# Optimization experiments

Hardware: AMD Instinct MI355X
Metric: run time of the kernel (lower is better)

Reference implementation:

```python
import jax, jax.numpy as jnp
import numpy as np
import math

B, T, C = 2, 1024, 1024
NEMBD = 1024
NATTN = 1024
NHEAD = 16
CTX = 1024
HS = NATTN // NHEAD          # head size = 64
ROT = HS // 2                # rotary dims = 32


def rotate_half(x):
    x1, x2 = x[..., : x.shape[-1] // 2], x[..., x.shape[-1] // 2 :]
    return jnp.concatenate((-x2, x1), axis=-1)


def setup_inputs() -> dict:
    key = jax.random.key(0)
    ks = jax.random.split(key, 16)
    s = 0.02
    inp = {
        "x": jax.random.normal(ks[0], (B, T, C), dtype=jnp.float32),
        # time-decay params (torch inits them to ones; add noise for a nontrivial test)
        "time_w": 1.0 + s * jax.random.normal(ks[1], (NHEAD, CTX), dtype=jnp.float32),
        "time_alpha": 1.0 + s * jax.random.normal(ks[2], (NHEAD, 1, CTX), dtype=jnp.float32),
        "time_beta": 1.0 + s * jax.random.normal(ks[3], (NHEAD, CTX, 1), dtype=jnp.float32),
        "time_gamma": 1.0 + s * jax.random.normal(ks[4], (CTX, 1), dtype=jnp.float32),
        # projections (stored as (in, out) for x @ W)
        "Wq": s * jax.random.normal(ks[5], (NEMBD, NATTN), dtype=jnp.float32),
        "bq": s * jax.random.normal(ks[6], (NATTN,), dtype=jnp.float32),
        "Wk": s * jax.random.normal(ks[7], (NEMBD, NATTN), dtype=jnp.float32),
        "bk": s * jax.random.normal(ks[8], (NATTN,), dtype=jnp.float32),
        "Wv": s * jax.random.normal(ks[9], (NEMBD, NATTN), dtype=jnp.float32),
        "bv": s * jax.random.normal(ks[10], (NATTN,), dtype=jnp.float32),
        # 1x1 conv over head channels: (out_head, in_head)
        "Wmix": s * jax.random.normal(ks[11], (NHEAD, NHEAD), dtype=jnp.float32),
        "Wo": s * jax.random.normal(ks[12], (NATTN, NEMBD), dtype=jnp.float32),
        "bo": s * jax.random.normal(ks[13], (NEMBD,), dtype=jnp.float32),
    }
    return inp


def reference(x, time_w, time_alpha, time_beta, time_gamma,
              Wq, bq, Wk, bk, Wv, bv, Wmix, Wo, bo):
    Bx, Tx, Cx = x.shape
    TT = CTX

    # --- relative time-decay weight matrix (H, T, T) ---
    w = jnp.pad(time_w, ((0, 0), (0, TT)))          # (H, 2TT)
    w = jnp.tile(w, (1, TT))                        # (H, 2TT*TT)
    w = w[:, :-TT].reshape(NHEAD, TT, 2 * TT - 1)
    w = w[:, :, TT - 1:]                            # (H, TT, TT)
    w = w[:, :Tx, :Tx] * time_alpha[:, :, :Tx] * time_beta[:, :Tx, :]

    # --- time shift of the first half of channels ---
    half = Cx // 2
    x_shift = jnp.pad(x[:, :, :half], ((0, 0), (1, 0), (0, 0)))[:, :Tx, :]
    xs = jnp.concatenate([x_shift, x[:, :, half:]], axis=-1)

    # --- q/k/v projections -> (B, H, T, hs) ---
    q = (xs @ Wq + bq).reshape(Bx, Tx, NHEAD, HS).transpose(0, 2, 1, 3)
    k = (xs @ Wk + bk).reshape(Bx, Tx, NHEAD, HS).transpose(0, 2, 1, 3)
    v = (xs @ Wv + bv).reshape(Bx, Tx, NHEAD, HS).transpose(0, 2, 1, 3)

    # --- rotary on the first ROT dims of each head (base = ctx_len) ---
    qr, q_pass = q[..., :ROT], q[..., ROT:]
    kr, k_pass = k[..., :ROT], k[..., ROT:]
    inv_freq = 1.0 / (jnp.float32(CTX) ** (jnp.arange(0, ROT, 2, dtype=jnp.float32) / ROT))
    t = jnp.arange(Tx, dtype=jnp.float32)
    freqs = t[:, None] * inv_freq[None, :]          # (T, ROT/2)
    emb = jnp.concatenate((freqs, freqs), axis=-1)  # (T, ROT)
    cos, sin = jnp.cos(emb), jnp.sin(emb)
    qr = qr * cos + rotate_half(qr) * sin
    kr = kr * cos + rotate_half(kr) * sin
    q = jnp.concatenate((qr, q_pass), axis=-1)
    k = jnp.concatenate((kr, k_pass), axis=-1)

    # --- attention with time decay and cross-head 1x1 mix ---
    att = jnp.einsum('bhtd,bhsd->bhts', q, k) * (1.0 / math.sqrt(HS))
    att = jax.nn.softmax(att, axis=-1)
    att = att * w[None]                              # (B,H,T,T) * (1,H,T,T)
    att = jnp.einsum('gh,bhts->bgts', Wmix, att)     # 1x1 conv over head channel
    y = jnp.einsum('bhts,bhsd->bhtd', att, v)
    y = y.transpose(0, 2, 1, 3).reshape(Bx, Tx, NATTN)
    return (y @ Wo + bo) * time_gamma[:Tx, :]
```

## Files before the change

kernel.cpp:

```cpp
#include <hip/hip_runtime.h>

typedef unsigned short u16;
typedef unsigned int u32;
typedef __attribute__((ext_vector_type(8))) short bf16x8;
typedef __attribute__((ext_vector_type(4))) float f32x4;

#define MFMA(a,b,c) __builtin_amdgcn_mfma_f32_16x16x32_bf16(a,b,c,0,0,0)

__device__ __forceinline__ float b2f(u16 u){
  union { unsigned int i; float f; } v; v.i = ((unsigned int)u)<<16; return v.f;
}
__device__ __forceinline__ u16 f2b(float f){
  union { float f; unsigned int i; } v; v.f = f;
  unsigned int r = (v.i + 0x7FFFu + ((v.i>>16)&1u))>>16;
  return (u16)r;
}
__device__ __forceinline__ void gld16(const u16* g, u16* l){
  __builtin_amdgcn_global_load_lds((const __attribute__((address_space(1))) u32*)g,
                                   (__attribute__((address_space(3))) u32*)l, 16, 0, 0);
}

__global__ __launch_bounds__(256) void k_pre(
    const float* __restrict__ x,
    const float* __restrict__ Wq, const float* __restrict__ Wk,
    const float* __restrict__ Wv, const float* __restrict__ Wo,
    u16* __restrict__ xs, u16* __restrict__ WT, u16* __restrict__ WoT)
{
  int bid = blockIdx.x;
  int tid = threadIdx.x;
  if (bid < 1024){
    int idx = bid*256 + tid;
    size_t e = (size_t)idx*8;
    int c = (int)(e & 1023);
    int t = (int)((e>>10)&1023);
    float4 f0 = {0.f,0.f,0.f,0.f}, f1 = {0.f,0.f,0.f,0.f};
    const float* src = nullptr;
    if (c < 512){ if (t > 0) src = x + e - 1024; }
    else        { src = x + e; }
    if (src){ f0 = *(const float4*)src; f1 = *(const float4*)(src+4); }
    u16 o[8];
    o[0]=f2b(f0.x); o[1]=f2b(f0.y); o[2]=f2b(f0.z); o[3]=f2b(f0.w);
    o[4]=f2b(f1.x); o[5]=f2b(f1.y); o[6]=f2b(f1.z); o[7]=f2b(f1.w);
    *(uint4*)(xs + e) = *(const uint4*)o;
    return;
  }
  int z  = (bid-1024)>>8;
  int rc = (bid-1024)&255;
  const float* src = (z==0)?Wq:((z==1)?Wk:((z==2)?Wv:Wo));
  u16* dst = (z==3)? WoT : (WT + (size_t)z*1048576);
  int c0 = (rc&15)*64, r0 = (rc>>4)*64;
  __shared__ u16 tile[64][72];
  int r = tid>>2, cc = (tid&3)*16;
  const float* sp = src + (size_t)(r0+r)*1024 + c0+cc;
  float4 a0 = *(const float4*)(sp);
  float4 a1 = *(const float4*)(sp+4);
  float4 a2 = *(const float4*)(sp+8);
  float4 a3 = *(const float4*)(sp+12);
  tile[r][cc+0]=f2b(a0.x); tile[r][cc+1]=f2b(a0.y); tile[r][cc+2]=f2b(a0.z); tile[r][cc+3]=f2b(a0.w);
  tile[r][cc+4]=f2b(a1.x); tile[r][cc+5]=f2b(a1.y); tile[r][cc+6]=f2b(a1.z); tile[r][cc+7]=f2b(a1.w);
  tile[r][cc+8]=f2b(a2.x); tile[r][cc+9]=f2b(a2.y); tile[r][cc+10]=f2b(a2.z); tile[r][cc+11]=f2b(a2.w);
  tile[r][cc+12]=f2b(a3.x); tile[r][cc+13]=f2b(a3.y); tile[r][cc+14]=f2b(a3.z); tile[r][cc+15]=f2b(a3.w);
  __syncthreads();
  int c = tid>>2, rr = (tid&3)*16;
  uint4 o0,o1; u16* p0=(u16*)&o0; u16* p1=(u16*)&o1;
  #pragma unroll
  for (int i=0;i<8;i++){ p0[i]=tile[rr+i][c]; p1[i]=tile[rr+8+i][c]; }
  *(uint4*)(dst + (size_t)(c0+c)*1024 + r0+rr)   = o0;
  *(uint4*)(dst + (size_t)(c0+c)*1024 + r0+rr+8) = o1;
}

__global__ __launch_bounds__(256) void k_gemm_qkv(
    const u16* __restrict__ A, const u16* __restrict__ Bt,
    const float* __restrict__ bq, const float* __restrict__ bk, const float* __restrict__ bv,
    u16* __restrict__ qb, u16* __restrict__ kb, u16* __restrict__ vT)
{
  __shared__ u16 As[128*32];
  __shared__ u16 Bs[64*32];
  const int n0 = blockIdx.x*64, m0 = blockIdx.y*128;
  const int tid = threadIdx.x, lane = tid&63, wave = tid>>6;
  const int quad = lane>>4, l16 = lane&15;
  const int wm = (wave>>1)*64, wn = (wave&1)*32;
  f32x4 zero = {0.f,0.f,0.f,0.f};
  f32x4 acc[4][2];
  #pragma unroll
  for (int i=0;i<4;i++){ acc[i][0]=zero; acc[i][1]=zero; }
  const int srow = (lane>>2), scol = (lane&3)*8;
  const u16* pa0 = A  + (size_t)(m0 + wave*16 + srow)*1024 + scol;
  const u16* pb0 = Bt + (size_t)(n0 + wave*16 + srow)*1024 + scol;
  u16* lA0 = &As[(wave*16)*32];
  u16* lA1 = &As[(64 + wave*16)*32];
  u16* lB0 = &Bs[(wave*16)*32];
  for (int k0=0;k0<1024;k0+=32){
    __syncthreads();
    gld16(pa0 + k0,           lA0);
    gld16(pa0 + 64*1024 + k0, lA1);
    gld16(pb0 + k0,           lB0);
    __syncthreads();
    bf16x8 af[4], bfr[2];
    #pragma unroll
    for (int mt=0;mt<4;mt++) af[mt]  = *(const bf16x8*)&As[(wm+mt*16+l16)*32 + quad*8];
    #pragma unroll
    for (int nt=0;nt<2;nt++) bfr[nt] = *(const bf16x8*)&Bs[(wn+nt*16+l16)*32 + quad*8];
    #pragma unroll
    for (int mt=0;mt<4;mt++){
      acc[mt][0] = MFMA(af[mt], bfr[0], acc[mt][0]);
      acc[mt][1] = MFMA(af[mt], bfr[1], acc[mt][1]);
    }
  }
  const int which = n0>>10;
  const int nn0 = (n0 & 1023) + wn;
  const int h = (n0 & 1023)>>6;
  const float* barr = (which==0)?bq:((which==1)?bk:bv);
  float bias0 = barr[nn0 + l16];
  float bias1 = barr[nn0 + 16 + l16];
  if (which == 2){
    #pragma unroll
    for (int mt=0;mt<4;mt++)
      #pragma unroll
      for (int r=0;r<4;r++){
        int m = m0 + wm + mt*16 + quad*4 + r;
        int bb = m>>10, t = m&1023;
        size_t base = (size_t)(bb*16+h)*65536 + t;
        int d0 = wn + l16;
        vT[base + (size_t)d0*1024]      = f2b(acc[mt][0][r] + bias0);
        vT[base + (size_t)(d0+16)*1024] = f2b(acc[mt][1][r] + bias1);
      }
  } else {
    const float scale = (which==0)?0.125f:1.0f;
    u16* dst = (which==0)? qb : kb;
    if (wn == 0){
      const float e = exp2f(-0.625f*(float)l16);
      #pragma unroll
      for (int mt=0;mt<4;mt++)
        #pragma unroll
        for (int r=0;r<4;r++){
          int m = m0 + wm + mt*16 + quad*4 + r;
          int bb = m>>10, t = m&1023;
          float f = (float)t * e;
          float cs = cosf(f), sn = sinf(f);
          float x0 = acc[mt][0][r] + bias0;
          float x1 = acc[mt][1][r] + bias1;
          float v0 = (x0*cs - x1*sn)*scale;
          float v1 = (x1*cs + x0*sn)*scale;
          size_t ob = (((size_t)(bb*16+h))*1024 + (size_t)t)*64 + l16;
          dst[ob]    = f2b(v0);
          dst[ob+16] = f2b(v1);
        }
    } else {
      #pragma unroll
      for (int mt=0;mt<4;mt++)
        #pragma unroll
        for (int r=0;r<4;r++){
          int m = m0 + wm + mt*16 + quad*4 + r;
          int bb = m>>10, t = m&1023;
          float v2 = (acc[mt][0][r] + bias0)*scale;
          float v3 = (acc[mt][1][r] + bias1)*scale;
          size_t ob = (((size_t)(bb*16+h))*1024 + (size_t)t)*64 + 32 + l16;
          dst[ob]    = f2b(v2);
          dst[ob+16] = f2b(v3);
        }
    }
  }
}

__global__ __launch_bounds__(256) void k_gemm_out(
    const u16* __restrict__ A, const u16* __restrict__ Bt,
    const float* __restrict__ bo, const float* __restrict__ gamma, float* __restrict__ out)
{
  __shared__ u16 As[128*32];
  __shared__ u16 Bs[64*32];
  const int n0 = blockIdx.x*64, m0 = blockIdx.y*128;
  const int tid = threadIdx.x, lane = tid&63, wave = tid>>6;
  const int quad = lane>>4, l16 = lane&15;
  const int wm = (wave>>1)*64, wn = (wave&1)*32;
  f32x4 zero = {0.f,0.f,0.f,0.f};
  f32x4 acc[4][2];
  #pragma unroll
  for (int i=0;i<4;i++){ acc[i][0]=zero; acc[i][1]=zero; }
  const int srow = (lane>>2), scol = (lane&3)*8;
  const u16* pa0 = A  + (size_t)(m0 + wave*16 + srow)*1024 + scol;
  const u16* pb0 = Bt + (size_t)(n0 + wave*16 + srow)*1024 + scol;
  u16* lA0 = &As[(wave*16)*32];
  u16* lA1 = &As[(64 + wave*16)*32];
  u16* lB0 = &Bs[(wave*16)*32];
  for (int k0=0;k0<1024;k0+=32){
    __syncthreads();
    gld16(pa0 + k0,           lA0);
    gld16(pa0 + 64*1024 + k0, lA1);
    gld16(pb0 + k0,           lB0);
    __syncthreads();
    bf16x8 af[4], bfr[2];
    #pragma unroll
    for (int mt=0;mt<4;mt++) af[mt]  = *(const bf16x8*)&As[(wm+mt*16+l16)*32 + quad*8];
    #pragma unroll
    for (int nt=0;nt<2;nt++) bfr[nt] = *(const bf16x8*)&Bs[(wn+nt*16+l16)*32 + quad*8];
    #pragma unroll
    for (int mt=0;mt<4;mt++){
      acc[mt][0] = MFMA(af[mt], bfr[0], acc[mt][0]);
      acc[mt][1] = MFMA(af[mt], bfr[1], acc[mt][1]);
    }
  }
  #pragma unroll
  for (int nt=0;nt<2;nt++){
    int colg = n0 + wn + nt*16 + l16;
    float bias = bo[colg];
    #pragma unroll
    for (int mt=0;mt<4;mt++)
      #pragma unroll
      for (int r=0;r<4;r++){
        int m = m0 + wm + mt*16 + quad*4 + r;
        int t = m&1023;
        float val = (acc[mt][nt][r] + bias)*gamma[t];
        out[(size_t)m*1024 + colg] = val;
      }
  }
}

__global__ __launch_bounds__(1024) void k_sm(
    const u16* __restrict__ q, const u16* __restrict__ k,
    const float* __restrict__ tw, const float* __restrict__ alpha, const float* __restrict__ beta,
    u16* __restrict__ P)
{
  const int tb = blockIdx.x, h = blockIdx.y, b = blockIdx.z;
  const int t0b = tb*64;
  const int tid = threadIdx.x;
  const int wave = tid>>6, lane = tid&63, quad = lane>>4, l16 = lane&15;
  const int wt = wave>>2, ws = wave&3;

  __shared__ u16 qs[64*76];
  __shared__ u16 ks[256*76];
  __shared__ float tws[1024];
  __shared__ float als[1024];
  __shared__ float pm[4][64];
  __shared__ float pl[4][64];
  __shared__ float fm[64];
  __shared__ float fr[64];

  const size_t bh = (size_t)(b*16+h)*65536;
  const u16* qp = q + bh;
  const u16* kp = k + bh;

  if (tid < 512){
    int row = tid>>3, g = tid&7;
    *(uint4*)&qs[row*76 + g*8] = *(const uint4*)(qp + (size_t)(t0b+row)*64 + g*8);
  }
  tws[tid] = tw[h*1024 + tid];
  als[tid] = alpha[h*1024 + tid];
  __syncthreads();

  bf16x8 qf0 = *(const bf16x8*)&qs[(wt*16+l16)*76 + quad*8];
  bf16x8 qf1 = *(const bf16x8*)&qs[(wt*16+l16)*76 + quad*8 + 32];

  f32x4 acc[16];
  #pragma unroll
  for (int i=0;i<16;i++){ acc[i][0]=0.f; acc[i][1]=0.f; acc[i][2]=0.f; acc[i][3]=0.f; }

  #pragma unroll
  for (int c=0;c<4;c++){
    if (c) __syncthreads();
    {
      int row = tid>>3, g = tid&7;
      *(uint4*)&ks[row*76 + g*8]       = *(const uint4*)(kp + (size_t)(c*256+row)*64 + g*8);
      *(uint4*)&ks[(row+128)*76 + g*8] = *(const uint4*)(kp + (size_t)(c*256+row+128)*64 + g*8);
    }
    __syncthreads();
    #pragma unroll
    for (int j=0;j<4;j++){
      int lt = j*4 + ws;
      bf16x8 kf0 = *(const bf16x8*)&ks[(lt*16+l16)*76 + quad*8];
      bf16x8 kf1 = *(const bf16x8*)&ks[(lt*16+l16)*76 + quad*8 + 32];
      acc[c*4+j] = MFMA(qf0, kf0, acc[c*4+j]);
      acc[c*4+j] = MFMA(qf1, kf1, acc[c*4+j]);
    }
  }

  float mrow[4], lrow[4];
  #pragma unroll
  for (int r=0;r<4;r++){
    float m = acc[0][r];
    #pragma unroll
    for (int a=1;a<16;a++) m = fmaxf(m, acc[a][r]);
    #pragma unroll
    for (int off=1; off<16; off<<=1) m = fmaxf(m, __shfl_xor(m, off));
    float l = 0.f;
    #pragma unroll
    for (int a=0;a<16;a++) l += __expf(acc[a][r]-m);
    #pragma unroll
    for (int off=1; off<16; off<<=1) l += __shfl_xor(l, off);
    mrow[r]=m; lrow[r]=l;
  }
  if (l16==0){
    #pragma unroll
    for (int r=0;r<4;r++){
      pm[ws][wt*16+quad*4+r] = mrow[r];
      pl[ws][wt*16+quad*4+r] = lrow[r];
    }
  }
  __syncthreads();
  if (tid < 64){
    float m0s = pm[0][tid], m1s = pm[1][tid], m2s = pm[2][tid], m3s = pm[3][tid];
    float m = fmaxf(fmaxf(m0s,m1s), fmaxf(m2s,m3s));
    float l = pl[0][tid]*__expf(m0s-m) + pl[1][tid]*__expf(m1s-m)
            + pl[2][tid]*__expf(m2s-m) + pl[3][tid]*__expf(m3s-m);
    fm[tid] = m;
    fr[tid] = beta[h*1024 + t0b + tid] / l;
  }
  __syncthreads();

  u16* Pp = P + (((size_t)b)<<24) + (((size_t)h)<<10);
  float m_f[4], r_f[4]; int trow[4];
  #pragma unroll
  for (int r=0;r<4;r++){
    int rg = wt*16+quad*4+r;
    m_f[r] = fm[rg]; r_f[r] = fr[rg]; trow[r] = t0b + rg;
  }
  const int slim = tb*4 + wt;
  #pragma unroll
  for (int c=0;c<4;c++)
    #pragma unroll
    for (int j=0;j<4;j++){
      int st = c*16 + j*4 + ws;
      if (st > slim) continue;
      int s = st*16 + l16;
      float av = als[s];
      #pragma unroll
      for (int r=0;r<4;r++){
        int t = trow[r];
        float p = 0.f;
        if (s <= t)
          p = __expf(acc[c*4+j][r]-m_f[r])*r_f[r]*tws[1023+s-t]*av;
        Pp[((size_t)t<<14) + s] = f2b(p);
      }
    }
}

__global__ __launch_bounds__(256) void k_mix(const u16* __restrict__ P, const float* __restrict__ Wm,
                                             u16* __restrict__ Ab)
{
  const int t = blockIdx.x, b = blockIdx.y;
  const int tid = threadIdx.x;
  const int g = tid>>4, sg = tid&15;
  __shared__ u16 Ps[16*264];
  float w[16];
  #pragma unroll
  for (int h=0;h<16;h++) w[h] = Wm[g*16+h];
  const int tmaxr = t|15;
  const int ncw = (t>>8) + 1;
  const size_t slab = (((size_t)b)<<24) + (((size_t)t)<<14);
  const u16* pp = P + slab;
  u16* ap = Ab + slab;
  for (int c=0;c<ncw;c++){
    int s0 = c*256;
    if (s0 <= tmaxr){
      if (c) __syncthreads();
      int colg = sg*16;
      uint4 z = {0u,0u,0u,0u};
      uint4 v0 = z, v1 = z;
      if (s0+colg <= tmaxr){
        v0 = *(const uint4*)(pp + ((size_t)g<<10) + s0+colg);
        v1 = *(const uint4*)(pp + ((size_t)g<<10) + s0+colg+8);
      }
      *(uint4*)&Ps[g*264+colg]   = v0;
      *(uint4*)&Ps[g*264+colg+8] = v1;
      __syncthreads();
      float acc[16];
      #pragma unroll
      for (int i=0;i<16;i++) acc[i]=0.f;
      #pragma unroll
      for (int h=0;h<16;h++){
        float wh = w[h];
        #pragma unroll
        for (int j=0;j<4;j++){
          ushort4 u = *(const ushort4*)&Ps[h*264 + sg*16 + j*4];
          acc[j*4+0] += wh*b2f(u.x);
          acc[j*4+1] += wh*b2f(u.y);
          acc[j*4+2] += wh*b2f(u.z);
          acc[j*4+3] += wh*b2f(u.w);
        }
      }
      u16 o[16];
      #pragma unroll
      for (int i=0;i<16;i++) o[i] = f2b(acc[i]);
      *(uint4*)(ap + ((size_t)g<<10) + s0 + sg*16)     = *(uint4*)&o[0];
      *(uint4*)(ap + ((size_t)g<<10) + s0 + sg*16 + 8) = *(uint4*)&o[8];
    } else {
      uint4 z = {0u,0u,0u,0u};
      *(uint4*)(ap + ((size_t)g<<10) + s0 + sg*16)     = z;
      *(uint4*)(ap + ((size_t)g<<10) + s0 + sg*16 + 8) = z;
    }
  }
}

__global__ __launch_bounds__(1024) void k_pv(const u16* __restrict__ Ab, const u16* __restrict__ vT,
                                             u16* __restrict__ y)
{
  const int tb = blockIdx.x;
  const int bg = blockIdx.y;
  const int b = bg>>4, g = bg&15;
  const int t0b = tb*64;
  const int tid = threadIdx.x;
  const int wave = tid>>6, lane = tid&63, quad = lane>>4, l16 = lane&15;
  const int wt = wave>>2, wd = wave&3;
  __shared__ u16 As[64*264];
  __shared__ u16 Vs[64*264];
  const u16* ap = Ab + (((size_t)b)<<24) + ((size_t)g<<10);
  const u16* vp = vT + (size_t)bg*65536;
  f32x4 acc = {0.f,0.f,0.f,0.f};
  const int nc = tb/4 + 1;
  const int row = tid>>4, col = (tid&15)*16;
  for (int c=0;c<nc;c++){
    if (c) __syncthreads();
    int s0 = c*256;
    *(uint4*)&As[row*264+col]   = *(const uint4*)(ap + ((size_t)(t0b+row)<<14) + s0+col);
    *(uint4*)&As[row*264+col+8] = *(const uint4*)(ap + ((size_t)(t0b+row)<<14) + s0+col+8);
    *(uint4*)&Vs[row*264+col]   = *(const uint4*)(vp + (size_t)row*1024 + s0+col);
    *(uint4*)&Vs[row*264+col+8] = *(const uint4*)(vp + (size_t)row*1024 + s0+col+8);
    __syncthreads();
    #pragma unroll
    for (int ks=0;ks<8;ks++){
      bf16x8 af  = *(const bf16x8*)&As[(wt*16+l16)*264 + ks*32 + quad*8];
      bf16x8 bfv = *(const bf16x8*)&Vs[(wd*16+l16)*264 + ks*32 + quad*8];
      acc = MFMA(af, bfv, acc);
    }
  }
  #pragma unroll
  for (int r=0;r<4;r++){
    int t = t0b + wt*16 + quad*4 + r;
    y[(size_t)(b*1024+t)*1024 + g*64 + wd*16 + l16] = f2b(acc[r]);
  }
}

__global__ void k_fail(float* out){ if (threadIdx.x==0) out[0] = 1e30f; }

extern "C" void kernel_launch(void* const* d_in, const int* in_sizes, int n_in,
                              void* d_out, int out_size, void* d_ws, size_t ws_size,
                              hipStream_t stream)
{
  const float* x     = (const float*)d_in[0];
  const float* tw    = (const float*)d_in[1];
  const float* alpha = (const float*)d_in[2];
  const float* beta  = (const float*)d_in[3];
  const float* gamma = (const float*)d_in[4];
  const float* Wq    = (const float*)d_in[5];
  const float* bq    = (const float*)d_in[6];
  const float* Wk    = (const float*)d_in[7];
  const float* bk    = (const float*)d_in[8];
  const float* Wv    = (const float*)d_in[9];
  const float* bv    = (const float*)d_in[10];
  const float* Wmix  = (const float*)d_in[11];
  const float* Wo    = (const float*)d_in[12];
  const float* bo    = (const float*)d_in[13];
  float* out = (float*)d_out;

  char* ws = (char*)d_ws;
  size_t off = 0;
  auto take = [&](size_t bytes)->char*{
    char* p = ws + off; off += (bytes + 255) & ~(size_t)255; return p;
  };
  u16*   xs  = (u16*)take((size_t)2097152*2);
  u16*   WT  = (u16*)take((size_t)3145728*2);
  u16*   WoT = (u16*)take((size_t)1048576*2);
  u16*   qb  = (u16*)take((size_t)2097152*2);
  u16*   kb  = (u16*)take((size_t)2097152*2);
  u16*   vTb = (u16*)take((size_t)2097152*2);
  u16*   yb  = (u16*)take((size_t)2097152*2);
  u16*   P   = (u16*)take((size_t)33554432*2);
  u16*   A   = (u16*)take((size_t)33554432*2);
  if (off > ws_size){
    hipLaunchKernelGGL(k_fail, dim3(1), dim3(64), 0, stream, out);
    return;
  }

  hipLaunchKernelGGL(k_pre, dim3(2048), dim3(256), 0, stream,
                     x, Wq, Wk, Wv, Wo, xs, WT, WoT);
  hipLaunchKernelGGL(k_gemm_qkv, dim3(48,16), dim3(256), 0, stream,
                     xs, WT, bq, bk, bv, qb, kb, vTb);
  hipLaunchKernelGGL(k_sm, dim3(16,16,2), dim3(1024), 0, stream,
                     qb, kb, tw, alpha, beta, P);
  hipLaunchKernelGGL(k_mix, dim3(1024,2), dim3(256), 0, stream, P, Wmix, A);
  hipLaunchKernelGGL(k_pv, dim3(16,32), dim3(1024), 0, stream, A, vTb, yb);
  hipLaunchKernelGGL(k_gemm_out, dim3(16,16), dim3(256), 0, stream, yb, WoT, bo, gamma, out);
}
```

Measured before the change: 211.7 us.

## Stage softmax P through LDS for coalesced stores, skip masked tiles, shrink out-GEMM tile

The softmax kernel now writes each probability tile into shared memory (reusing the k buffer) and then stores coalesced 16-element rows to global memory, replacing scattered 2-byte stores. The mix kernel no longer writes zeros for column blocks above the causal limit, and the PV kernel reads A only where it lies inside the causal region, substituting zeros otherwise. The output GEMM tile drops from 128 to 64 rows, doubling the grid for better CU occupancy. Together these aim to cut global memory traffic and raise store efficiency, at the cost of extra barriers in the softmax kernel and reliance on LDS reuse being safe.

```diff
diff --git a/kernel.cpp b/kernel.cpp
--- a/kernel.cpp
+++ b/kernel.cpp
@@ -167,35 +167,33 @@
     const u16* __restrict__ A, const u16* __restrict__ Bt,
     const float* __restrict__ bo, const float* __restrict__ gamma, float* __restrict__ out)
 {
-  __shared__ u16 As[128*32];
+  __shared__ u16 As[64*32];
   __shared__ u16 Bs[64*32];
-  const int n0 = blockIdx.x*64, m0 = blockIdx.y*128;
+  const int n0 = blockIdx.x*64, m0 = blockIdx.y*64;
   const int tid = threadIdx.x, lane = tid&63, wave = tid>>6;
   const int quad = lane>>4, l16 = lane&15;
-  const int wm = (wave>>1)*64, wn = (wave&1)*32;
+  const int wm = (wave>>1)*32, wn = (wave&1)*32;
   f32x4 zero = {0.f,0.f,0.f,0.f};
-  f32x4 acc[4][2];
-  #pragma unroll
-  for (int i=0;i<4;i++){ acc[i][0]=zero; acc[i][1]=zero; }
+  f32x4 acc[2][2];
+  #pragma unroll
+  for (int i=0;i<2;i++){ acc[i][0]=zero; acc[i][1]=zero; }
   const int srow = (lane>>2), scol = (lane&3)*8;
   const u16* pa0 = A  + (size_t)(m0 + wave*16 + srow)*1024 + scol;
   const u16* pb0 = Bt + (size_t)(n0 + wave*16 + srow)*1024 + scol;
   u16* lA0 = &As[(wave*16)*32];
-  u16* lA1 = &As[(64 + wave*16)*32];
   u16* lB0 = &Bs[(wave*16)*32];
   for (int k0=0;k0<1024;k0+=32){
     __syncthreads();
-    gld16(pa0 + k0,           lA0);
-    gld16(pa0 + 64*1024 + k0, lA1);
-    gld16(pb0 + k0,           lB0);
-    __syncthreads();
-    bf16x8 af[4], bfr[2];
-    #pragma unroll
-    for (int mt=0;mt<4;mt++) af[mt]  = *(const bf16x8*)&As[(wm+mt*16+l16)*32 + quad*8];
+    gld16(pa0 + k0, lA0);
+    gld16(pb0 + k0, lB0);
+    __syncthreads();
+    bf16x8 af[2], bfr[2];
+    #pragma unroll
+    for (int mt=0;mt<2;mt++) af[mt]  = *(const bf16x8*)&As[(wm+mt*16+l16)*32 + quad*8];
     #pragma unroll
     for (int nt=0;nt<2;nt++) bfr[nt] = *(const bf16x8*)&Bs[(wn+nt*16+l16)*32 + quad*8];
     #pragma unroll
-    for (int mt=0;mt<4;mt++){
+    for (int mt=0;mt<2;mt++){
       acc[mt][0] = MFMA(af[mt], bfr[0], acc[mt][0]);
       acc[mt][1] = MFMA(af[mt], bfr[1], acc[mt][1]);
     }
@@ -205,7 +203,7 @@
     int colg = n0 + wn + nt*16 + l16;
     float bias = bo[colg];
     #pragma unroll
-    for (int mt=0;mt<4;mt++)
+    for (int mt=0;mt<2;mt++)
       #pragma unroll
       for (int r=0;r<4;r++){
         int m = m0 + wm + mt*16 + quad*4 + r;
@@ -315,23 +313,40 @@
     m_f[r] = fm[rg]; r_f[r] = fr[rg]; trow[r] = t0b + rg;
   }
   const int slim = tb*4 + wt;
-  #pragma unroll
-  for (int c=0;c<4;c++)
+  u16* Pb = ks;
+  const int srowP = tid>>4;
+  const int sgu = tid&15;
+  const int tglob = t0b + srowP;
+  const int tmax = tglob|15;
+  const int ncP = tb/4 + 1;
+  for (int c=0;c<ncP;c++){
+    __syncthreads();
     #pragma unroll
     for (int j=0;j<4;j++){
       int st = c*16 + j*4 + ws;
       if (st > slim) continue;
       int s = st*16 + l16;
+      int s_loc = (j*4+ws)*16 + l16;
       float av = als[s];
       #pragma unroll
       for (int r=0;r<4;r++){
-        int t = trow[r];
+        int t = trow[r], t_loc = wt*16 + quad*4 + r;
         float p = 0.f;
         if (s <= t)
           p = __expf(acc[c*4+j][r]-m_f[r])*r_f[r]*tws[1023+s-t]*av;
-        Pp[((size_t)t<<14) + s] = f2b(p);
+        Pb[t_loc*264 + s_loc] = f2b(p);
       }
     }
+    __syncthreads();
+    int sg0 = c*256 + sgu*16;
+    if (sg0 <= tmax){
+      uint4 a0 = *(const uint4*)&Pb[srowP*264 + sgu*16];
+      uint4 a1 = *(const uint4*)&Pb[srowP*264 + sgu*16 + 8];
+      u16* dst = Pp + (((size_t)tglob)<<14) + sg0;
+      *(uint4*)(dst)   = a0;
+      *(uint4*)(dst+8) = a1;
+    }
+  }
 }
 
 __global__ __launch_bounds__(256) void k_mix(const u16* __restrict__ P, const float* __restrict__ Wm,
@@ -351,43 +366,38 @@
   u16* ap = Ab + slab;
   for (int c=0;c<ncw;c++){
     int s0 = c*256;
-    if (s0 <= tmaxr){
-      if (c) __syncthreads();
-      int colg = sg*16;
-      uint4 z = {0u,0u,0u,0u};
-      uint4 v0 = z, v1 = z;
-      if (s0+colg <= tmaxr){
-        v0 = *(const uint4*)(pp + ((size_t)g<<10) + s0+colg);
-        v1 = *(const uint4*)(pp + ((size_t)g<<10) + s0+colg+8);
+    if (c) __syncthreads();
+    int colg = sg*16;
+    uint4 z = {0u,0u,0u,0u};
+    uint4 v0 = z, v1 = z;
+    if (s0+colg <= tmaxr){
+      v0 = *(const uint4*)(pp + ((size_t)g<<10) + s0+colg);
+      v1 = *(const uint4*)(pp + ((size_t)g<<10) + s0+colg+8);
+    }
+    *(uint4*)&Ps[g*264+colg]   = v0;
+    *(uint4*)&Ps[g*264+colg+8] = v1;
+    __syncthreads();
+    if (s0 + sg*16 > tmaxr) continue;
+    float acc[16];
+    #pragma unroll
+    for (int i=0;i<16;i++) acc[i]=0.f;
+    #pragma unroll
+    for (int h=0;h<16;h++){
+      float wh = w[h];
+      #pragma unroll
+      for (int j=0;j<4;j++){
+        ushort4 u = *(const ushort4*)&Ps[h*264 + sg*16 + j*4];
+        acc[j*4+0] += wh*b2f(u.x);
+        acc[j*4+1] += wh*b2f(u.y);
+        acc[j*4+2] += wh*b2f(u.z);
+        acc[j*4+3] += wh*b2f(u.w);
       }
-      *(uint4*)&Ps[g*264+colg]   = v0;
-      *(uint4*)&Ps[g*264+colg+8] = v1;
-      __syncthreads();
-      float acc[16];
-      #pragma unroll
-      for (int i=0;i<16;i++) acc[i]=0.f;
-      #pragma unroll
-      for (int h=0;h<16;h++){
-        float wh = w[h];
-        #pragma unroll
-        for (int j=0;j<4;j++){
-          ushort4 u = *(const ushort4*)&Ps[h*264 + sg*16 + j*4];
-          acc[j*4+0] += wh*b2f(u.x);
-          acc[j*4+1] += wh*b2f(u.y);
-          acc[j*4+2] += wh*b2f(u.z);
-          acc[j*4+3] += wh*b2f(u.w);
-        }
-      }
-      u16 o[16];
-      #pragma unroll
-      for (int i=0;i<16;i++) o[i] = f2b(acc[i]);
-      *(uint4*)(ap + ((size_t)g<<10) + s0 + sg*16)     = *(uint4*)&o[0];
-      *(uint4*)(ap + ((size_t)g<<10) + s0 + sg*16 + 8) = *(uint4*)&o[8];
-    } else {
-      uint4 z = {0u,0u,0u,0u};
-      *(uint4*)(ap + ((size_t)g<<10) + s0 + sg*16)     = z;
-      *(uint4*)(ap + ((size_t)g<<10) + s0 + sg*16 + 8) = z;
-    }
+    }
+    u16 o[16];
+    #pragma unroll
+    for (int i=0;i<16;i++) o[i] = f2b(acc[i]);
+    *(uint4*)(ap + ((size_t)g<<10) + s0 + sg*16)     = *(uint4*)&o[0];
+    *(uint4*)(ap + ((size_t)g<<10) + s0 + sg*16 + 8) = *(uint4*)&o[8];
   }
 }
 
@@ -408,11 +418,19 @@
   f32x4 acc = {0.f,0.f,0.f,0.f};
   const int nc = tb/4 + 1;
   const int row = tid>>4, col = (tid&15)*16;
+  const int trow_g = t0b + row;
+  const int tmax = trow_g|15;
   for (int c=0;c<nc;c++){
     if (c) __syncthreads();
     int s0 = c*256;
-    *(uint4*)&As[row*264+col]   = *(const uint4*)(ap + ((size_t)(t0b+row)<<14) + s0+col);
-    *(uint4*)&As[row*264+col+8] = *(const uint4*)(ap + ((size_t)(t0b+row)<<14) + s0+col+8);
+    uint4 z = {0u,0u,0u,0u};
+    uint4 a0 = z, a1 = z;
+    if (s0 + col <= tmax){
+      a0 = *(const uint4*)(ap + ((size_t)trow_g<<14) + s0+col);
+      a1 = *(const uint4*)(ap + ((size_t)trow_g<<14) + s0+col+8);
+    }
+    *(uint4*)&As[row*264+col]   = a0;
+    *(uint4*)&As[row*264+col+8] = a1;
     *(uint4*)&Vs[row*264+col]   = *(const uint4*)(vp + (size_t)row*1024 + s0+col);
     *(uint4*)&Vs[row*264+col+8] = *(const uint4*)(vp + (size_t)row*1024 + s0+col+8);
     __syncthreads();
@@ -479,5 +497,5 @@
                      qb, kb, tw, alpha, beta, P);
   hipLaunchKernelGGL(k_mix, dim3(1024,2), dim3(256), 0, stream, P, Wmix, A);
   hipLaunchKernelGGL(k_pv, dim3(16,32), dim3(1024), 0, stream, A, vTb, yb);
-  hipLaunchKernelGGL(k_gemm_out, dim3(16,16), dim3(256), 0, stream, yb, WoT, bo, gamma, out);
-}
+  hipLaunchKernelGGL(k_gemm_out, dim3(16,32), dim3(256), 0, stream, yb, WoT, bo, gamma, out);
+}
```

After: 280.3 us. +32.4%, slower.
